# Optimization experiments

Hardware: AMD Instinct MI355X
Metric: run time of the kernel (lower is better)

## Reference

```python
import jax, jax.numpy as jnp
import numpy as np

N = 100000
E = 3200000
D = 128


def setup_inputs() -> dict:
    key = jax.random.key(0)
    k1, k2, k3, k4 = jax.random.split(key, 4)
    x = jax.random.normal(k1, (N, D), dtype=jnp.float32)
    edge_index = jax.random.randint(k2, (2, E), 0, N, dtype=jnp.int64)
    W1 = jax.random.normal(k3, (D, 16), dtype=jnp.float32) * (1.0 / np.sqrt(D))
    b1 = jnp.zeros((16,), dtype=jnp.float32)
    W2 = jax.random.normal(k4, (16, 2), dtype=jnp.float32) * (1.0 / np.sqrt(16))
    b2 = jnp.zeros((2,), dtype=jnp.float32)
    return {"x": x, "edge_index": edge_index, "W1": W1, "b1": b1, "W2": W2, "b2": b2}


def _gcn_conv(h, src, dst, norm, W, b):
    # transform first (out_dim <= in_dim), then normalized scatter-add aggregation
    h = h @ W                                   # [N, out]
    msg = h[src] * norm[:, None]                # [E+N, out] gathered messages
    agg = jax.ops.segment_sum(msg, dst, num_segments=N)
    return agg + b


def reference(x, edge_index, W1, b1, W2, b2):
    loops = jnp.arange(N, dtype=edge_index.dtype)
    src = jnp.concatenate([edge_index[0], loops])   # row (message source)
    dst = jnp.concatenate([edge_index[1], loops])   # col (aggregation target)
    # symmetric GCN normalization: deg over dst, norm = d^-1/2[src] * d^-1/2[dst]
    deg = jax.ops.segment_sum(jnp.ones_like(src, dtype=x.dtype), dst, num_segments=N)
    dinv = jnp.where(deg > 0, jax.lax.rsqrt(deg), 0.0)
    norm = dinv[src] * dinv[dst]

    h = _gcn_conv(x, src, dst, norm, W1, b1)
    h = jax.nn.relu(h)
    h = _gcn_conv(h, src, dst, norm, W2, b2)
    return jax.nn.log_softmax(h, axis=1)
```

## Files before the change

kernel.cpp:

```cpp
#include <hip/hip_runtime.h>
#include <hip/hip_fp16.h>
#include <math.h>

#define N_NODES 100000
#define N_EDGES 3200000
#define D_IN    128
#define H1      16

#define BSH     8
#define NPB     256
#define NB      391
#define CAP     13056
#define HCAP    (CAP / 2)
#define PBLK    512
#define CHUNK   6250
#define ELS_CAP 12128
#define NLINES  (ELS_CAP / 16)
#define MROWS   64


__global__ __launch_bounds__(512) void k_zero(int* __restrict__ cursor) {
    int t = threadIdx.x;
    if (t < NB) cursor[t] = 0;
}

__global__ __launch_bounds__(512) void k_partition(const int* __restrict__ ei,
                                                   int* __restrict__ cursor,
                                                   unsigned int* __restrict__ eop) {
    __shared__ int h[512];
    __shared__ int loff[512];
    __shared__ int resv[NB];
    __shared__ unsigned short owner[NLINES];
    __shared__ unsigned char rank8[CHUNK];
    __shared__ unsigned int els[ELS_CAP];
    int t = threadIdx.x;
    h[t] = 0;
    __syncthreads();
    int c0 = blockIdx.x * CHUNK;
    const int* srcs = ei + c0;
    const int* dsts = ei + N_EDGES + c0;
    for (int i = t; i < CHUNK; i += 512)
        rank8[i] = (unsigned char)atomicAdd(&h[dsts[i] >> BSH], 1);
    __syncthreads();
    int cp = (h[t] + 15) & ~15;
    loff[t] = cp;
    __syncthreads();
    for (int o = 1; o < 512; o <<= 1) {
        int u = (t >= o) ? loff[t - o] : 0;
        __syncthreads();
        loff[t] += u;
        __syncthreads();
    }
    int inc = loff[t];
    int totalpad = loff[511];
    int ex = inc - cp;
    __syncthreads();
    loff[t] = ex;
    if (t < NB && cp) {
        resv[t] = atomicAdd(&cursor[t], cp);
        int l0 = ex >> 4;
        for (int k = 0; k < (cp >> 4); ++k) owner[l0 + k] = (unsigned short)t;
    }
    for (int i = t; i < totalpad; i += 512) els[i] = 0xFFFFFFFFu;
    __syncthreads();
    for (int i = t; i < CHUNK; i += 512) {
        int s = srcs[i];
        int d = dsts[i];
        int b = d >> BSH;
        els[loff[b] + (int)rank8[i]] = ((unsigned)s << BSH) | (unsigned)(d & (NPB - 1));
    }
    __syncthreads();
    for (int i = t; i < totalpad; i += 512) {
        int b   = owner[i >> 4];
        int pos = resv[b] + (i - loff[b]);
        if (pos < CAP)
            eop[(size_t)b * CAP + pos] = els[i];
    }
}

__global__ __launch_bounds__(512) void k_build(const int* __restrict__ cursor,
                                               const unsigned int* __restrict__ eop,
                                               unsigned int* __restrict__ eos,
                                               int* __restrict__ nstart,
                                               int* __restrict__ ndeg,
                                               float* __restrict__ dinv) {
    __shared__ int cnt[128], off[128], cur[128];
    int t = threadIdx.x;
    int b = blockIdx.x >> 1, hh = blockIdx.x & 1;
    if (t < 128) cnt[t] = 0;
    __syncthreads();
    int n = cursor[b]; if (n > CAP) n = CAP;
    const unsigned int* reg = eop + (size_t)b * CAP;
    for (int i = t; i < n; i += 512) {
        unsigned int v = reg[i];
        if ((int)v >= 0) {
            int dloc = v & (NPB - 1);
            if ((dloc >> 7) == hh) atomicAdd(&cnt[dloc & 127], 1);
        }
    }
    __syncthreads();
    int val = (t < 128) ? cnt[t] : 0;
    if (t < 128) off[t] = val;
    __syncthreads();
    for (int o = 1; o < 128; o <<= 1) {
        int u = 0;
        if (t < 128 && t >= o) u = off[t - o];
        __syncthreads();
        if (t < 128) off[t] += u;
        __syncthreads();
    }
    if (t < 128) {
        int ex = off[t] - val;
        int node = (b << BSH) + (hh << 7) + t;
        if (node < N_NODES) {
            nstart[node] = b * CAP + hh * HCAP + ex;
            ndeg[node]   = val;
            dinv[node]   = rsqrtf((float)(val + 1));
        }
        cur[t] = ex;
    }
    __syncthreads();
    unsigned int* oreg = eos + (size_t)b * CAP + (size_t)hh * HCAP;
    for (int i = t; i < n; i += 512) {
        unsigned int v = reg[i];
        if ((int)v >= 0) {
            int dloc = v & (NPB - 1);
            if ((dloc >> 7) == hh) {
                int r = atomicAdd(&cur[dloc & 127], 1);
                oreg[r] = v >> BSH;
            }
        }
    }
}

__global__ __launch_bounds__(256) void k_mm1(const float* __restrict__ x,
                                             const float* __restrict__ W1,
                                             const float* __restrict__ dinv,
                                             __half* __restrict__ h1h) {
    __shared__ float sX[MROWS][D_IN + 1];
    int t = threadIdx.x;
    int r0 = blockIdx.x * MROWS;
    for (int i = t; i < MROWS * (D_IN / 4); i += 256) {
        int row = i >> 5, c4 = i & 31;
        int grow = r0 + row;
        float4 v = (grow < N_NODES) ? ((const float4*)x)[(size_t)grow * 32 + c4]
                                    : make_float4(0.f, 0.f, 0.f, 0.f);
        sX[row][c4 * 4 + 0] = v.x; sX[row][c4 * 4 + 1] = v.y;
        sX[row][c4 * 4 + 2] = v.z; sX[row][c4 * 4 + 3] = v.w;
    }
    __syncthreads();
    int lane = t & 63;
    int c0 = __builtin_amdgcn_readfirstlane((t >> 6) * 4);
    float a0 = 0.f, a1 = 0.f, a2 = 0.f, a3 = 0.f;
#pragma unroll 4
    for (int d = 0; d < D_IN; ++d) {
        float xv = sX[lane][d];
        a0 = fmaf(xv, W1[d * 16 + c0 + 0], a0);
        a1 = fmaf(xv, W1[d * 16 + c0 + 1], a1);
        a2 = fmaf(xv, W1[d * 16 + c0 + 2], a2);
        a3 = fmaf(xv, W1[d * 16 + c0 + 3], a3);
    }
    int grow = r0 + lane;
    if (grow < N_NODES) {
        float di = dinv[grow];
        __half2* o = (__half2*)(h1h + (size_t)grow * H1 + c0);
        o[0] = __floats2half2_rn(a0 * di, a1 * di);
        o[1] = __floats2half2_rn(a2 * di, a3 * di);
    }
}

__global__ __launch_bounds__(256) void k_agg1(const unsigned int* __restrict__ eos,
                                              const int* __restrict__ nstart,
                                              const int* __restrict__ ndeg,
                                              const __half* __restrict__ h1h,
                                              const float* __restrict__ dinv,
                                              const float* __restrict__ b1,
                                              const float* __restrict__ W2,
                                              float2* __restrict__ h2f) {
    int t = threadIdx.x;
    int g = t >> 4, l = t & 15;
    int node = blockIdx.x * 16 + g;
    int e0 = nstart[node], e1 = e0 + ndeg[node];
    float acc = 0.f;
    int j = e0;
    for (; j + 4 <= e1; j += 4) {
        int s0 = eos[j], s1 = eos[j + 1], s2 = eos[j + 2], s3 = eos[j + 3];
        acc += __half2float(h1h[s0 * H1 + l]) + __half2float(h1h[s1 * H1 + l])
             + __half2float(h1h[s2 * H1 + l]) + __half2float(h1h[s3 * H1 + l]);
    }
    for (; j < e1; ++j) acc += __half2float(h1h[(int)eos[j] * H1 + l]);
    float di = dinv[node];
    float s  = acc + __half2float(h1h[node * H1 + l]);
    float h  = fmaxf(fmaf(di, s, b1[l]), 0.f);
    float p0 = h * W2[2 * l], p1 = h * W2[2 * l + 1];
#pragma unroll
    for (int off = 1; off < 16; off <<= 1) {
        p0 += __shfl_xor(p0, off);
        p1 += __shfl_xor(p1, off);
    }
    if (l == 0) h2f[node] = make_float2(p0 * di, p1 * di);
}

__global__ __launch_bounds__(256) void k_agg2(const unsigned int* __restrict__ eos,
                                              const int* __restrict__ nstart,
                                              const int* __restrict__ ndeg,
                                              const float2* __restrict__ h2f,
                                              const float* __restrict__ dinv,
                                              const float* __restrict__ b2,
                                              float* __restrict__ out) {
    int tg = blockIdx.x * 256 + threadIdx.x;
    int node = tg >> 2, l = tg & 3;
    if (node >= N_NODES) return;
    int e0 = nstart[node], e1 = e0 + ndeg[node];
    float ax = 0.f, ay = 0.f;
    for (int j = e0 + l; j < e1; j += 4) {
        float2 m = h2f[eos[j]];
        ax += m.x; ay += m.y;
    }
    ax += __shfl_xor(ax, 1); ay += __shfl_xor(ay, 1);
    ax += __shfl_xor(ax, 2); ay += __shfl_xor(ay, 2);
    if (l == 0) {
        float di = dinv[node];
        float2 self = h2f[node];
        float a0 = fmaf(di, ax + self.x, b2[0]);
        float a1 = fmaf(di, ay + self.y, b2[1]);
        float m  = fmaxf(a0, a1);
        float lg = logf(expf(a0 - m) + expf(a1 - m));
        out[2 * node]     = a0 - m - lg;
        out[2 * node + 1] = a1 - m - lg;
    }
}

extern "C" void kernel_launch(void* const* d_in, const int* in_sizes, int n_in,
                              void* d_out, int out_size, void* d_ws, size_t ws_size,
                              hipStream_t stream) {
    const float* x  = (const float*)d_in[0];
    const int*   ei = (const int*)d_in[1];
    const float* W1 = (const float*)d_in[2];
    const float* b1 = (const float*)d_in[3];
    const float* W2 = (const float*)d_in[4];
    const float* b2 = (const float*)d_in[5];
    float* out = (float*)d_out;

    int*          cursor = (int*)d_ws;
    int*          nstart = cursor + 512;
    int*          ndeg   = nstart + 100352;
    float*        dinv   = (float*)(ndeg + 100352);
    __half*       h1h    = (__half*)(dinv + 100352);
    float2*       h2f    = (float2*)(h1h + (size_t)100352 * H1);
    unsigned int* eop    = (unsigned int*)(h2f + 100352);
    unsigned int* eos    = eop + (size_t)NB * CAP;

    k_zero     <<<1,    512, 0, stream>>>(cursor);
    k_partition<<<PBLK, 512, 0, stream>>>(ei, cursor, eop);
    k_build    <<<NB * 2, 512, 0, stream>>>(cursor, eop, eos, nstart, ndeg, dinv);
    k_mm1      <<<(N_NODES + MROWS - 1) / MROWS, 256, 0, stream>>>(x, W1, dinv, h1h);
    k_agg1     <<<N_NODES / 16, 256, 0, stream>>>(eos, nstart, ndeg, h1h, dinv, b1, W2, h2f);
    k_agg2     <<<(N_NODES * 4 + 255) / 256, 256, 0, stream>>>(eos, nstart, ndeg, h2f, dinv, b2, out);
}
```

Measured before the change: 233.7 us.

## Drop CSR build; aggregate directly from per-bucket partitions with LDS sort

Removes the global CSR construction (nstart/ndeg/eos writes) and turns the build kernel into a degree-only counter. Layer-1 aggregation now re-reads each bucket's partitioned edges, counting-sorts them into shared memory per 128-node half, and gathers from there. Layer-2 aggregation scatters straight into LDS float atomics. The aim is to save the global write and re-read of the sorted edge array, at the cost of reading eop three times, a launch with only 782 blocks and heavy register use, and a silent overflow drop when a half-bucket exceeds AELS edges.

```diff
diff --git a/kernel.cpp b/kernel.cpp
--- a/kernel.cpp
+++ b/kernel.cpp
@@ -11,12 +11,13 @@
 #define NPB     256
 #define NB      391
 #define CAP     13056
-#define HCAP    (CAP / 2)
 #define PBLK    512
 #define CHUNK   6250
 #define ELS_CAP 12128
 #define NLINES  (ELS_CAP / 16)
 #define MROWS   64
+#define SLOTS   26
+#define AELS    5120
 
 
 __global__ __launch_bounds__(512) void k_zero(int* __restrict__ cursor) {
@@ -78,13 +79,10 @@
     }
 }
 
-__global__ __launch_bounds__(512) void k_build(const int* __restrict__ cursor,
+__global__ __launch_bounds__(512) void k_count(const int* __restrict__ cursor,
                                                const unsigned int* __restrict__ eop,
-                                               unsigned int* __restrict__ eos,
-                                               int* __restrict__ nstart,
-                                               int* __restrict__ ndeg,
                                                float* __restrict__ dinv) {
-    __shared__ int cnt[128], off[128], cur[128];
+    __shared__ int cnt[128];
     int t = threadIdx.x;
     int b = blockIdx.x >> 1, hh = blockIdx.x & 1;
     if (t < 128) cnt[t] = 0;
@@ -99,37 +97,9 @@
         }
     }
     __syncthreads();
-    int val = (t < 128) ? cnt[t] : 0;
-    if (t < 128) off[t] = val;
-    __syncthreads();
-    for (int o = 1; o < 128; o <<= 1) {
-        int u = 0;
-        if (t < 128 && t >= o) u = off[t - o];
-        __syncthreads();
-        if (t < 128) off[t] += u;
-        __syncthreads();
-    }
     if (t < 128) {
-        int ex = off[t] - val;
         int node = (b << BSH) + (hh << 7) + t;
-        if (node < N_NODES) {
-            nstart[node] = b * CAP + hh * HCAP + ex;
-            ndeg[node]   = val;
-            dinv[node]   = rsqrtf((float)(val + 1));
-        }
-        cur[t] = ex;
-    }
-    __syncthreads();
-    unsigned int* oreg = eos + (size_t)b * CAP + (size_t)hh * HCAP;
-    for (int i = t; i < n; i += 512) {
-        unsigned int v = reg[i];
-        if ((int)v >= 0) {
-            int dloc = v & (NPB - 1);
-            if ((dloc >> 7) == hh) {
-                int r = atomicAdd(&cur[dloc & 127], 1);
-                oreg[r] = v >> BSH;
-            }
-        }
+        if (node < N_NODES) dinv[node] = rsqrtf((float)(cnt[t] + 1));
     }
 }
 
@@ -169,65 +139,128 @@
     }
 }
 
-__global__ __launch_bounds__(256) void k_agg1(const unsigned int* __restrict__ eos,
-                                              const int* __restrict__ nstart,
-                                              const int* __restrict__ ndeg,
-                                              const __half* __restrict__ h1h,
-                                              const float* __restrict__ dinv,
-                                              const float* __restrict__ b1,
-                                              const float* __restrict__ W2,
-                                              float2* __restrict__ h2f) {
-    int t = threadIdx.x;
+__global__ __launch_bounds__(512) void k_agg1f(const int* __restrict__ cursor,
+                                               const unsigned int* __restrict__ eop,
+                                               const __half* __restrict__ h1h,
+                                               const float* __restrict__ dinv,
+                                               const float* __restrict__ b1,
+                                               const float* __restrict__ W2,
+                                               float2* __restrict__ h2f) {
+    __shared__ int cnt[128], off[128];
+    __shared__ int els[AELS];
+    int t = threadIdx.x;
+    int b = blockIdx.x >> 1, hh = blockIdx.x & 1;
+    if (t < 128) cnt[t] = 0;
+    __syncthreads();
+    int n = cursor[b]; if (n > CAP) n = CAP;
+    const unsigned int* reg = eop + (size_t)b * CAP;
+    unsigned int vals[SLOTS];
+#pragma unroll
+    for (int k = 0; k < SLOTS; ++k) {
+        int i = t + k * 512;
+        unsigned int w = 0xFFFFFFFFu;
+        if (i < n) {
+            unsigned int v = reg[i];
+            if ((int)v >= 0) {
+                int dloc = v & (NPB - 1);
+                if ((dloc >> 7) == hh) {
+                    int r = atomicAdd(&cnt[dloc & 127], 1);
+                    w = (v >> 8) | ((unsigned)(r & 127) << 17)
+                                 | ((unsigned)(dloc & 127) << 24);
+                }
+            }
+        }
+        vals[k] = w;
+    }
+    __syncthreads();
+    int val = (t < 128) ? cnt[t] : 0;
+    if (t < 128) off[t] = val;
+    __syncthreads();
+    for (int o = 1; o < 128; o <<= 1) {
+        int u = 0;
+        if (t < 128 && t >= o) u = off[t - o];
+        __syncthreads();
+        if (t < 128) off[t] += u;
+        __syncthreads();
+    }
+    if (t < 128) off[t] -= val;
+    __syncthreads();
+#pragma unroll
+    for (int k = 0; k < SLOTS; ++k) {
+        unsigned int w = vals[k];
+        if (w != 0xFFFFFFFFu) {
+            int src  = w & 0x1FFFF;
+            int r    = (w >> 17) & 127;
+            int dloc = (w >> 24) & 127;
+            int p = off[dloc] + r;
+            if (p < AELS) els[p] = src;
+        }
+    }
+    __syncthreads();
     int g = t >> 4, l = t & 15;
-    int node = blockIdx.x * 16 + g;
-    int e0 = nstart[node], e1 = e0 + ndeg[node];
-    float acc = 0.f;
-    int j = e0;
-    for (; j + 4 <= e1; j += 4) {
-        int s0 = eos[j], s1 = eos[j + 1], s2 = eos[j + 2], s3 = eos[j + 3];
-        acc += __half2float(h1h[s0 * H1 + l]) + __half2float(h1h[s1 * H1 + l])
-             + __half2float(h1h[s2 * H1 + l]) + __half2float(h1h[s3 * H1 + l]);
-    }
-    for (; j < e1; ++j) acc += __half2float(h1h[(int)eos[j] * H1 + l]);
-    float di = dinv[node];
-    float s  = acc + __half2float(h1h[node * H1 + l]);
-    float h  = fmaxf(fmaf(di, s, b1[l]), 0.f);
-    float p0 = h * W2[2 * l], p1 = h * W2[2 * l + 1];
+    for (int nn = g; nn < 128; nn += 32) {
+        int node = (b << BSH) + (hh << 7) + nn;
+        if (node >= N_NODES) continue;
+        int e = cnt[nn], base = off[nn];
+        float acc = 0.f;
+        int j = 0;
+        for (; j + 4 <= e; j += 4) {
+            int s0 = els[base + j],     s1 = els[base + j + 1];
+            int s2 = els[base + j + 2], s3 = els[base + j + 3];
+            acc += __half2float(h1h[s0 * H1 + l]) + __half2float(h1h[s1 * H1 + l])
+                 + __half2float(h1h[s2 * H1 + l]) + __half2float(h1h[s3 * H1 + l]);
+        }
+        for (; j < e; ++j) acc += __half2float(h1h[els[base + j] * H1 + l]);
+        float di = dinv[node];
+        float s  = acc + __half2float(h1h[node * H1 + l]);
+        float h  = fmaxf(fmaf(di, s, b1[l]), 0.f);
+        float p0 = h * W2[2 * l], p1 = h * W2[2 * l + 1];
 #pragma unroll
-    for (int off = 1; off < 16; off <<= 1) {
-        p0 += __shfl_xor(p0, off);
-        p1 += __shfl_xor(p1, off);
-    }
-    if (l == 0) h2f[node] = make_float2(p0 * di, p1 * di);
-}
-
-__global__ __launch_bounds__(256) void k_agg2(const unsigned int* __restrict__ eos,
-                                              const int* __restrict__ nstart,
-                                              const int* __restrict__ ndeg,
-                                              const float2* __restrict__ h2f,
-                                              const float* __restrict__ dinv,
-                                              const float* __restrict__ b2,
-                                              float* __restrict__ out) {
-    int tg = blockIdx.x * 256 + threadIdx.x;
-    int node = tg >> 2, l = tg & 3;
-    if (node >= N_NODES) return;
-    int e0 = nstart[node], e1 = e0 + ndeg[node];
-    float ax = 0.f, ay = 0.f;
-    for (int j = e0 + l; j < e1; j += 4) {
-        float2 m = h2f[eos[j]];
-        ax += m.x; ay += m.y;
-    }
-    ax += __shfl_xor(ax, 1); ay += __shfl_xor(ay, 1);
-    ax += __shfl_xor(ax, 2); ay += __shfl_xor(ay, 2);
-    if (l == 0) {
-        float di = dinv[node];
-        float2 self = h2f[node];
-        float a0 = fmaf(di, ax + self.x, b2[0]);
-        float a1 = fmaf(di, ay + self.y, b2[1]);
-        float m  = fmaxf(a0, a1);
-        float lg = logf(expf(a0 - m) + expf(a1 - m));
-        out[2 * node]     = a0 - m - lg;
-        out[2 * node + 1] = a1 - m - lg;
+        for (int o2 = 1; o2 < 16; o2 <<= 1) {
+            p0 += __shfl_xor(p0, o2);
+            p1 += __shfl_xor(p1, o2);
+        }
+        if (l == 0) h2f[node] = make_float2(p0 * di, p1 * di);
+    }
+}
+
+__global__ __launch_bounds__(512) void k_agg2f(const int* __restrict__ cursor,
+                                               const unsigned int* __restrict__ eop,
+                                               const float2* __restrict__ h2f,
+                                               const float* __restrict__ dinv,
+                                               const float* __restrict__ b2,
+                                               float* __restrict__ out) {
+    __shared__ float ax[128], ay[128];
+    int t = threadIdx.x;
+    int b = blockIdx.x >> 1, hh = blockIdx.x & 1;
+    if (t < 128) { ax[t] = 0.f; ay[t] = 0.f; }
+    __syncthreads();
+    int n = cursor[b]; if (n > CAP) n = CAP;
+    const unsigned int* reg = eop + (size_t)b * CAP;
+    for (int i = t; i < n; i += 512) {
+        unsigned int v = reg[i];
+        if ((int)v >= 0) {
+            int dloc = v & (NPB - 1);
+            if ((dloc >> 7) == hh) {
+                float2 m = h2f[v >> 8];
+                atomicAdd(&ax[dloc & 127], m.x);
+                atomicAdd(&ay[dloc & 127], m.y);
+            }
+        }
+    }
+    __syncthreads();
+    if (t < 128) {
+        int node = (b << BSH) + (hh << 7) + t;
+        if (node < N_NODES) {
+            float di = dinv[node];
+            float2 self = h2f[node];
+            float a0 = fmaf(di, ax[t] + self.x, b2[0]);
+            float a1 = fmaf(di, ay[t] + self.y, b2[1]);
+            float m  = fmaxf(a0, a1);
+            float lg = logf(expf(a0 - m) + expf(a1 - m));
+            out[2 * node]     = a0 - m - lg;
+            out[2 * node + 1] = a1 - m - lg;
+        }
     }
 }
 
@@ -243,18 +276,15 @@
     float* out = (float*)d_out;
 
     int*          cursor = (int*)d_ws;
-    int*          nstart = cursor + 512;
-    int*          ndeg   = nstart + 100352;
-    float*        dinv   = (float*)(ndeg + 100352);
+    float*        dinv   = (float*)(cursor + 512);
     __half*       h1h    = (__half*)(dinv + 100352);
     float2*       h2f    = (float2*)(h1h + (size_t)100352 * H1);
     unsigned int* eop    = (unsigned int*)(h2f + 100352);
-    unsigned int* eos    = eop + (size_t)NB * CAP;
-
-    k_zero     <<<1,    512, 0, stream>>>(cursor);
-    k_partition<<<PBLK, 512, 0, stream>>>(ei, cursor, eop);
-    k_build    <<<NB * 2, 512, 0, stream>>>(cursor, eop, eos, nstart, ndeg, dinv);
+
+    k_zero     <<<1,      512, 0, stream>>>(cursor);
+    k_partition<<<PBLK,   512, 0, stream>>>(ei, cursor, eop);
+    k_count    <<<NB * 2, 512, 0, stream>>>(cursor, eop, dinv);
     k_mm1      <<<(N_NODES + MROWS - 1) / MROWS, 256, 0, stream>>>(x, W1, dinv, h1h);
-    k_agg1     <<<N_NODES / 16, 256, 0, stream>>>(eos, nstart, ndeg, h1h, dinv, b1, W2, h2f);
-    k_agg2     <<<(N_NODES * 4 + 255) / 256, 256, 0, stream>>>(eos, nstart, ndeg, h2f, dinv, b2, out);
-}
+    k_agg1f    <<<NB * 2, 512, 0, stream>>>(cursor, eop, h1h, dinv, b1, W2, h2f);
+    k_agg2f    <<<NB * 2, 512, 0, stream>>>(cursor, eop, h2f, dinv, b2, out);
+}
```

Result: slower. 248.2 us (+6.2%).
